# Kernel optimization log

Measured on AMD Instinct MI355X. Metric: run time of the kernel, lower is better.

The kernel has to match this reference:

```python
import jax, jax.numpy as jnp
import numpy as np

EMBED = 512
EXPAND = 1024


def setup_inputs() -> dict:
    key = jax.random.key(0)
    k1, k2, k3, k4, k5 = jax.random.split(key, 5)
    B, C, P, N = 4, EMBED, 16, 1024
    x = jax.random.normal(k1, (B, C, P, N), dtype=jnp.float32)
    # 1x1 conv weights == per-pixel linear maps over the channel dim
    Wqkv = jax.random.normal(k2, (1 + 2 * EXPAND, C), dtype=jnp.float32) * (1.0 / np.sqrt(C))
    bqkv = jax.random.normal(k3, (1 + 2 * EXPAND,), dtype=jnp.float32) * 0.01
    Wout = jax.random.normal(k4, (C, EXPAND), dtype=jnp.float32) * (1.0 / np.sqrt(EXPAND))
    bout = jax.random.normal(k5, (C,), dtype=jnp.float32) * 0.01
    return {"x": x, "Wqkv": Wqkv, "bqkv": bqkv, "Wout": Wout, "bout": bout}


def reference(x, Wqkv, bqkv, Wout, bout):
    # qkv 1x1 conv: (B,C,P,N) -> (B, 1+2E, P, N)
    qkv = jnp.einsum('oc,bcpn->bopn', Wqkv, x) + bqkv[None, :, None, None]
    E = EXPAND
    query = qkv[:, :1]            # (B,1,P,N)
    key_t = qkv[:, 1:1 + E]       # (B,E,P,N)
    value = qkv[:, 1 + E:]        # (B,E,P,N)
    # softmax over patches dim (last axis); attn_dropout p=0.0 -> identity
    context_scores = jax.nn.softmax(query, axis=-1)
    # weighted sum over N, keepdim -> (B,E,P,1)
    context_vector = jnp.sum(key_t * context_scores, axis=-1, keepdims=True)
    # broadcast gate
    out = jax.nn.relu(value) * context_vector  # (B,E,P,N)
    # out 1x1 conv back to embed channels
    out = jnp.einsum('oe,bepn->bopn', Wout, out) + bout[None, :, None, None]
    return out
```

## Files before the change

### kernel.cpp

```cpp
#include <hip/hip_runtime.h>

#define EMBED 512
#define EXPAND 1024
#define PNUM 16
#define NLEN 1024
#define CHW (PNUM * NLEN)
#define SLABS 64

typedef unsigned short u16;
typedef unsigned int u32;
typedef __bf16 bf16x8 __attribute__((ext_vector_type(8)));
typedef u16 u16x8 __attribute__((ext_vector_type(8)));
typedef float f32x4 __attribute__((ext_vector_type(4)));

__device__ __forceinline__ u16 f2bf(float f) {
  u32 u = __builtin_bit_cast(u32, f);
  return (u16)((u + 0x7FFFu + ((u >> 16) & 1u)) >> 16);
}
__device__ __forceinline__ float bf2f(u16 h) {
  return __builtin_bit_cast(float, (u32)h << 16);
}
__device__ __forceinline__ void gld16(const u16* g, u16* l) {
  __builtin_amdgcn_global_load_lds((__attribute__((address_space(1))) void*)g,
                                   (__attribute__((address_space(3))) void*)l,
                                   16, 0, 0);
}
__device__ __forceinline__ f32x4 MFMA(bf16x8 a, bf16x8 b, f32x4 c) {
  return __builtin_amdgcn_mfma_f32_16x16x32_bf16(a, b, c, 0, 0, 0);
}

__global__ __launch_bounds__(256) void k_convert_w(
    const float* __restrict__ Wqkv, const float* __restrict__ Wout,
    u16* __restrict__ WvB, u16* __restrict__ WoutB) {
  const int NV = EXPAND * EMBED;
  int idx = (blockIdx.x * 256 + threadIdx.x) * 4;
  if (idx < NV) {
    float4 v = *(const float4*)(Wqkv + (size_t)(1 + EXPAND) * EMBED + idx);
    uint2 u = make_uint2((u32)f2bf(v.x) | ((u32)f2bf(v.y) << 16),
                         (u32)f2bf(v.z) | ((u32)f2bf(v.w) << 16));
    *(uint2*)(WvB + idx) = u;
  } else {
    int j = idx - NV;
    float4 v = *(const float4*)(Wout + j);
    uint2 u = make_uint2((u32)f2bf(v.x) | ((u32)f2bf(v.y) << 16),
                         (u32)f2bf(v.z) | ((u32)f2bf(v.w) << 16));
    *(uint2*)(WoutB + j) = u;
  }
}

__global__ __launch_bounds__(256) void k_convert_x(
    const float* __restrict__ x, const float* __restrict__ Wqkv,
    float* __restrict__ q, u16* __restrict__ xbT) {
  __shared__ __align__(16) u16 tile[128 * 64];
  __shared__ float qp[256 * 4];
  const int slab = blockIdx.x >> 3, nw = blockIdx.x & 7;
  const int b = slab >> 4, p = slab & 15;
  const int t = threadIdx.x;
  const int c8 = t & 7;
  const int ng = t >> 3;
  const float* xs = x + (size_t)b * (EMBED * CHW) + (size_t)p * NLEN + nw * 128;
  u16* dst = xbT + (size_t)slab * (NLEN * EMBED) + (size_t)(nw * 128) * EMBED;
  float qa[4] = {0.f, 0.f, 0.f, 0.f};

  for (int cc = 0; cc < 8; ++cc) {
    const int cbase = cc * 64;
    float4 v[8];
#pragma unroll
    for (int k = 0; k < 8; ++k)
      v[k] = *(const float4*)(xs + (size_t)(cbase + c8 * 8 + k) * CHW + ng * 4);
    const float* w0 = Wqkv + cbase + c8 * 8;
#pragma unroll
    for (int k = 0; k < 8; ++k) {
      qa[0] += w0[k] * v[k].x;
      qa[1] += w0[k] * v[k].y;
      qa[2] += w0[k] * v[k].z;
      qa[3] += w0[k] * v[k].w;
    }
#pragma unroll
    for (int j = 0; j < 4; ++j) {
      const int nl = ng * 4 + j;
      float e[8];
#pragma unroll
      for (int k = 0; k < 8; ++k)
        e[k] = (j == 0) ? v[k].x : (j == 1) ? v[k].y : (j == 2) ? v[k].z : v[k].w;
      uint4 pk;
      pk.x = (u32)f2bf(e[0]) | ((u32)f2bf(e[1]) << 16);
      pk.y = (u32)f2bf(e[2]) | ((u32)f2bf(e[3]) << 16);
      pk.z = (u32)f2bf(e[4]) | ((u32)f2bf(e[5]) << 16);
      pk.w = (u32)f2bf(e[6]) | ((u32)f2bf(e[7]) << 16);
      *(uint4*)(tile + nl * 64 + ((c8 ^ (nl & 7)) << 3)) = pk;
    }
    __syncthreads();
#pragma unroll
    for (int m = 0; m < 4; ++m) {
      const int s = m * 256 + t;
      const int nl = s >> 3, ch = s & 7;
      uint4 vv = *(const uint4*)(tile + nl * 64 + ((ch ^ (nl & 7)) << 3));
      *(uint4*)(dst + (size_t)nl * EMBED + cbase + ch * 8) = vv;
    }
    __syncthreads();
  }
  qp[t * 4 + 0] = qa[0];
  qp[t * 4 + 1] = qa[1];
  qp[t * 4 + 2] = qa[2];
  qp[t * 4 + 3] = qa[3];
  __syncthreads();
  if (t < 128) {
    float a = 0.f;
#pragma unroll
    for (int o = 0; o < 8; ++o) a += qp[((((t >> 2) << 3) + o) << 2) + (t & 3)];
    q[(size_t)slab * NLEN + nw * 128 + t] = a;
  }
}

__global__ __launch_bounds__(256) void k_attn1(
    const float* __restrict__ q, const u16* __restrict__ xbT,
    float* __restrict__ ypart) {
  __shared__ float red[4];
  __shared__ float sm[256];
  __shared__ float yp[4][512];
  const int slab = blockIdx.x >> 2, qr = blockIdx.x & 3;
  const int t = threadIdx.x, w = t >> 6, l = t & 63;
  const float* qrow = q + (size_t)slab * NLEN;

  float4 q4 = ((const float4*)qrow)[t];
  float m = fmaxf(fmaxf(q4.x, q4.y), fmaxf(q4.z, q4.w));
#pragma unroll
  for (int sh = 32; sh; sh >>= 1) m = fmaxf(m, __shfl_xor(m, sh, 64));
  if (l == 0) red[w] = m;
  __syncthreads();
  float gm = fmaxf(fmaxf(red[0], red[1]), fmaxf(red[2], red[3]));
  float s = __expf(q4.x - gm) + __expf(q4.y - gm) + __expf(q4.z - gm) + __expf(q4.w - gm);
#pragma unroll
  for (int sh = 32; sh; sh >>= 1) s += __shfl_xor(s, sh, 64);
  __syncthreads();
  if (l == 0) red[w] = s;
  __syncthreads();
  float gs = red[0] + red[1] + red[2] + red[3];
  sm[t] = __expf(qrow[qr * 256 + t] - gm) / gs;
  __syncthreads();

  float ya[8] = {0.f, 0.f, 0.f, 0.f, 0.f, 0.f, 0.f, 0.f};
  const u16* xs = xbT + (size_t)slab * (NLEN * EMBED) + (size_t)qr * 256 * EMBED;
  for (int ni = 0; ni < 64; ++ni) {
    const int nloc = ni * 4 + w;
    const float sc = sm[nloc];
    u16x8 v = *(const u16x8*)(xs + (size_t)nloc * EMBED + l * 8);
#pragma unroll
    for (int j = 0; j < 8; ++j) ya[j] += sc * bf2f(v[j]);
  }
#pragma unroll
  for (int j = 0; j < 8; ++j) yp[w][l * 8 + j] = ya[j];
  __syncthreads();
  for (int c = t; c < 512; c += 256)
    ypart[((size_t)slab * 4 + qr) * 512 + c] = yp[0][c] + yp[1][c] + yp[2][c] + yp[3][c];
}

__global__ __launch_bounds__(256) void k_attn2(
    const float* __restrict__ ypart, const float* __restrict__ Wqkv,
    const float* __restrict__ bqkv, float* __restrict__ cv) {
  __shared__ float yl[512];
  const int slab = blockIdx.x >> 2, ec = blockIdx.x & 3;
  const int t = threadIdx.x;
  const int e = ec * 256 + t;
  const float* yb = ypart + (size_t)slab * 4 * 512;
  for (int c = t; c < 512; c += 256)
    yl[c] = yb[c] + yb[512 + c] + yb[1024 + c] + yb[1536 + c];
  __syncthreads();
  const float* wk = Wqkv + (size_t)(1 + e) * EMBED;
  float a = 0.f;
#pragma unroll 4
  for (int c0 = 0; c0 < EMBED; c0 += 4) {
    float4 wv = *(const float4*)(wk + c0);
    a += wv.x * yl[c0] + wv.y * yl[c0 + 1] + wv.z * yl[c0 + 2] + wv.w * yl[c0 + 3];
  }
  cv[(size_t)slab * EXPAND + e] = a + bqkv[1 + e];
}

template <int K, int NT>
__device__ __forceinline__ void gemm256(const u16* __restrict__ Abase,
                                        const u16* __restrict__ Bbase,
                                        u16* lds, f32x4 (&acc)[8][4]) {
  const int t = threadIdx.x;
  const int w = t >> 6, l = t & 63;
  const int wr = w >> 2, wc = w & 3;
  const int lr = l & 15, lj = l >> 4;
  const int rowA0 = wr * 128 + lr;
  const int rowB0 = wc * 64 + lr;

  auto stage = [&](u16* dstBase, const u16* gBase, int kt) {
#pragma unroll
    for (int i = 0; i < 4; ++i) {
      const int s = i * 512 + t;
      const int row = s >> 3;
      const int pch = s & 7;
      gld16(gBase + (size_t)row * K + kt + ((pch ^ (row & 7)) << 3),
            dstBase + s * 8);
    }
  };
  auto rdA = [&](const u16* bufA, int mi, int kc) -> bf16x8 {
    const int row = rowA0 + mi * 16;
    const int ch = kc * 4 + lj;
    return *(const bf16x8*)(bufA + row * 64 + ((ch ^ (row & 7)) << 3));
  };
  auto rdB = [&](const u16* bufB, int ni, int kc) -> bf16x8 {
    const int row = rowB0 + ni * 16;
    const int ch = kc * 4 + lj;
    return *(const bf16x8*)(bufB + row * 64 + ((ch ^ (row & 7)) << 3));
  };

  stage(lds, Abase, 0);
  stage(lds + 16384, Bbase, 0);
  stage(lds + 32768, Abase, 64);
  stage(lds + 49152, Bbase, 64);
  asm volatile("s_waitcnt vmcnt(8)" ::: "memory");
  __builtin_amdgcn_s_barrier();
  __builtin_amdgcn_sched_barrier(0);

#pragma unroll 1
  for (int kt = 0; kt < NT; ++kt) {
    u16* bufA = lds + (kt & 1) * 32768;
    u16* bufB = bufA + 16384;
    const bool st = (kt + 2) < NT;
    const int kt2 = (kt + 2) * 64;
    bf16x8 a0[4][2], a1[4][2], b0[2][2], b1[2][2];

#pragma unroll
    for (int mi = 0; mi < 4; ++mi)
#pragma unroll
      for (int kc = 0; kc < 2; ++kc) a0[mi][kc] = rdA(bufA, mi, kc);
#pragma unroll
    for (int ni = 0; ni < 2; ++ni)
#pragma unroll
      for (int kc = 0; kc < 2; ++kc) b0[ni][kc] = rdB(bufB, ni, kc);
    __builtin_amdgcn_s_barrier();
    __builtin_amdgcn_sched_barrier(0);
    __builtin_amdgcn_s_setprio(1);
#pragma unroll
    for (int mi = 0; mi < 4; ++mi)
#pragma unroll
      for (int ni = 0; ni < 2; ++ni)
#pragma unroll
        for (int kc = 0; kc < 2; ++kc)
          acc[mi][ni] = MFMA(a0[mi][kc], b0[ni][kc], acc[mi][ni]);
    __builtin_amdgcn_s_setprio(0);
    __builtin_amdgcn_sched_barrier(0);
    __builtin_amdgcn_s_barrier();
    __builtin_amdgcn_sched_barrier(0);

#pragma unroll
    for (int ni = 0; ni < 2; ++ni)
#pragma unroll
      for (int kc = 0; kc < 2; ++kc) b1[ni][kc] = rdB(bufB, ni + 2, kc);
    __builtin_amdgcn_s_barrier();
    __builtin_amdgcn_sched_barrier(0);
    __builtin_amdgcn_s_setprio(1);
#pragma unroll
    for (int mi = 0; mi < 4; ++mi)
#pragma unroll
      for (int ni = 0; ni < 2; ++ni)
#pragma unroll
        for (int kc = 0; kc < 2; ++kc)
          acc[mi][ni + 2] = MFMA(a0[mi][kc], b1[ni][kc], acc[mi][ni + 2]);
    __builtin_amdgcn_s_setprio(0);
    __builtin_amdgcn_sched_barrier(0);
    __builtin_amdgcn_s_barrier();
    __builtin_amdgcn_sched_barrier(0);

#pragma unroll
    for (int mi = 0; mi < 4; ++mi)
#pragma unroll
      for (int kc = 0; kc < 2; ++kc) a1[mi][kc] = rdA(bufA, mi + 4, kc);
    if (st) stage(bufB, Bbase, kt2);
    __builtin_amdgcn_s_barrier();
    __builtin_amdgcn_sched_barrier(0);
    __builtin_amdgcn_s_setprio(1);
#pragma unroll
    for (int mi = 0; mi < 4; ++mi)
#pragma unroll
      for (int ni = 0; ni < 2; ++ni)
#pragma unroll
        for (int kc = 0; kc < 2; ++kc)
          acc[mi + 4][ni + 2] = MFMA(a1[mi][kc], b1[ni][kc], acc[mi + 4][ni + 2]);
    __builtin_amdgcn_s_setprio(0);
    __builtin_amdgcn_sched_barrier(0);
    __builtin_amdgcn_s_barrier();
    __builtin_amdgcn_sched_barrier(0);

    if (st) stage(bufA, Abase, kt2);
    __builtin_amdgcn_s_barrier();
    __builtin_amdgcn_sched_barrier(0);
    __builtin_amdgcn_s_setprio(1);
#pragma unroll
    for (int mi = 0; mi < 4; ++mi)
#pragma unroll
      for (int ni = 0; ni < 2; ++ni)
#pragma unroll
        for (int kc = 0; kc < 2; ++kc)
          acc[mi + 4][ni] = MFMA(a1[mi][kc], b0[ni][kc], acc[mi + 4][ni]);
    __builtin_amdgcn_s_setprio(0);
    __builtin_amdgcn_sched_barrier(0);
    if (st)
      asm volatile("s_waitcnt vmcnt(8)" ::: "memory");
    else
      asm volatile("s_waitcnt vmcnt(0)" ::: "memory");
    __builtin_amdgcn_s_barrier();
    __builtin_amdgcn_sched_barrier(0);
  }
}

__global__ __launch_bounds__(512, 2) void k_gemm1(
    const u16* __restrict__ xbT, const u16* __restrict__ WvB,
    const float* __restrict__ bqkv, const float* __restrict__ cv,
    u16* __restrict__ midT) {
  __shared__ __align__(16) u16 lds[65536];
  const int bid = blockIdx.x;
  const int xc = bid & 7, k = bid >> 3;
  const int te = k & 3;
  const int gg = ((k >> 2) << 3) | xc;
  const int slab = gg >> 2, tn = gg & 3;
  const u16* A = xbT + (size_t)slab * (NLEN * EMBED) + (size_t)tn * 256 * EMBED;
  const u16* B = WvB + (size_t)te * 256 * EMBED;
  f32x4 acc[8][4];
  const f32x4 z = {0.f, 0.f, 0.f, 0.f};
#pragma unroll
  for (int i = 0; i < 8; ++i)
#pragma unroll
    for (int j = 0; j < 4; ++j) acc[i][j] = z;
  gemm256<EMBED, 8>(A, B, lds, acc);

  const int t = threadIdx.x, w = t >> 6, l = t & 63;
  const int wr = w >> 2, wc = w & 3;
  const int lr = l & 15, lq4 = (l >> 4) * 4;
#pragma unroll
  for (int ni = 0; ni < 4; ++ni) {
    const int col = wc * 64 + ni * 16 + lr;
    const int e = te * 256 + col;
    const float bv = bqkv[1 + EXPAND + e];
    const float cve = cv[(size_t)slab * EXPAND + e];
#pragma unroll
    for (int mi = 0; mi < 8; ++mi) {
      const int nr = wr * 128 + mi * 16 + lq4;
#pragma unroll
      for (int r = 0; r < 4; ++r) {
        float v = acc[mi][ni][r] + bv;
        v = v > 0.f ? v * cve : 0.f;
        const int row = nr + r;
        lds[row * 256 + ((((col >> 3) ^ (row & 7)) << 3) | (col & 7))] = f2bf(v);
      }
    }
  }
  __syncthreads();
  u16* mt = midT + (size_t)slab * (NLEN * EXPAND) + (size_t)te * 256;
#pragma unroll
  for (int it = 0; it < 16; ++it) {
    const int row = w * 32 + it * 2 + (l >> 5);
    const int ch = (l & 31) ^ (row & 7);
    uint4 v = *(const uint4*)(lds + row * 256 + ch * 8);
    *(uint4*)(mt + (size_t)(tn * 256 + row) * EXPAND + (l & 31) * 8) = v;
  }
}

__global__ __launch_bounds__(512, 2) void k_gemm2(
    const u16* __restrict__ midT, const u16* __restrict__ WoutB,
    const float* __restrict__ bout, float* __restrict__ out) {
  __shared__ __align__(16) u16 lds[65536];
  const int bid = blockIdx.x;
  const int xc = bid & 7, k = bid >> 3;
  const int to = k & 1;
  const int gg = ((k >> 1) << 3) | xc;
  const int slab = gg >> 2, tn = gg & 3;
  const int b = slab >> 4, p = slab & 15;
  const u16* A = midT + (size_t)slab * (NLEN * EXPAND) + (size_t)tn * 256 * EXPAND;
  const u16* B = WoutB + (size_t)to * 256 * EXPAND;
  f32x4 acc[8][4];
  const f32x4 z = {0.f, 0.f, 0.f, 0.f};
#pragma unroll
  for (int i = 0; i < 8; ++i)
#pragma unroll
    for (int j = 0; j < 4; ++j) acc[i][j] = z;
  gemm256<EXPAND, 16>(A, B, lds, acc);

  const int t = threadIdx.x, w = t >> 6, l = t & 63;
  const int wr = w >> 2, wc = w & 3;
  const int lr = l & 15, lq4 = (l >> 4) * 4;
  float* ob = out + (size_t)b * (EMBED * CHW) + (size_t)p * NLEN;
#pragma unroll
  for (int ni = 0; ni < 4; ++ni) {
    const int o = to * 256 + wc * 64 + ni * 16 + lr;
    const float bo = bout[o];
#pragma unroll
    for (int mi = 0; mi < 8; ++mi) {
      const int nr = tn * 256 + wr * 128 + mi * 16 + lq4;
      float4 v;
      v.x = acc[mi][ni][0] + bo;
      v.y = acc[mi][ni][1] + bo;
      v.z = acc[mi][ni][2] + bo;
      v.w = acc[mi][ni][3] + bo;
      *(float4*)(ob + (size_t)o * CHW + nr) = v;
    }
  }
}

extern "C" void kernel_launch(void* const* d_in, const int* in_sizes, int n_in,
                              void* d_out, int out_size, void* d_ws, size_t ws_size,
                              hipStream_t stream) {
  const float* x = (const float*)d_in[0];
  const float* Wqkv = (const float*)d_in[1];
  const float* bqkv = (const float*)d_in[2];
  const float* Wout = (const float*)d_in[3];
  const float* bout = (const float*)d_in[4];
  float* out = (float*)d_out;

  char* ws = (char*)d_ws;
  u16* xbT = (u16*)ws;
  u16* WvB = (u16*)(ws + 67108864);
  u16* WoutB = (u16*)(ws + 68157440);
  float* q = (float*)(ws + 69206016);
  float* cv = (float*)(ws + 69468160);
  u16* midT = (u16*)(ws + 69730304);
  float* ypart = (float*)(ws + 69730304);

  k_convert_w<<<1024, 256, 0, stream>>>(Wqkv, Wout, WvB, WoutB);
  k_convert_x<<<512, 256, 0, stream>>>(x, Wqkv, q, xbT);
  k_attn1<<<256, 256, 0, stream>>>(q, xbT, ypart);
  k_attn2<<<256, 256, 0, stream>>>(ypart, Wqkv, bqkv, cv);
  k_gemm1<<<1024, 512, 0, stream>>>(xbT, WvB, bqkv, cv, midT);
  k_gemm2<<<512, 512, 0, stream>>>(midT, WoutB, bout, out);
}
```

Before: 267.7 us.

## Switch GEMMs to 32x32x16 MFMA with swapped operands and direct epilogue stores

Both bf16 GEMMs move from the 16x16x32 to the 32x32x16 MFMA instruction, so each wave holds four 32x32 accumulator blocks instead of thirty-two 16x16 blocks. The weight matrix becomes operand A and the activations operand B, which removes the LDS transpose and the extra barrier in gemm1's epilogue. gemm1 now writes midT directly with small strided stores, and gemm2 writes the output row by row with coalesced scalar stores. Weight conversion is moved after attn1 so it can reuse the q buffer for a copy of the value bias, and several sched_barriers are dropped. The risk is less coalesced global writes in gemm1's epilogue and looser instruction scheduling.

```diff
diff --git a/kernel.cpp b/kernel.cpp
--- a/kernel.cpp
+++ b/kernel.cpp
@@ -12,6 +12,7 @@
 typedef __bf16 bf16x8 __attribute__((ext_vector_type(8)));
 typedef u16 u16x8 __attribute__((ext_vector_type(8)));
 typedef float f32x4 __attribute__((ext_vector_type(4)));
+typedef float f32x16 __attribute__((ext_vector_type(16)));
 
 __device__ __forceinline__ u16 f2bf(float f) {
   u32 u = __builtin_bit_cast(u32, f);
@@ -25,13 +26,14 @@
                                    (__attribute__((address_space(3))) void*)l,
                                    16, 0, 0);
 }
-__device__ __forceinline__ f32x4 MFMA(bf16x8 a, bf16x8 b, f32x4 c) {
-  return __builtin_amdgcn_mfma_f32_16x16x32_bf16(a, b, c, 0, 0, 0);
+__device__ __forceinline__ f32x16 MFMA32(bf16x8 a, bf16x8 b, f32x16 c) {
+  return __builtin_amdgcn_mfma_f32_32x32x16_bf16(a, b, c, 0, 0, 0);
 }
 
 __global__ __launch_bounds__(256) void k_convert_w(
     const float* __restrict__ Wqkv, const float* __restrict__ Wout,
-    u16* __restrict__ WvB, u16* __restrict__ WoutB) {
+    const float* __restrict__ bqkv, u16* __restrict__ WvB,
+    u16* __restrict__ WoutB, float* __restrict__ bvv) {
   const int NV = EXPAND * EMBED;
   int idx = (blockIdx.x * 256 + threadIdx.x) * 4;
   if (idx < NV) {
@@ -46,6 +48,10 @@
                          (u32)f2bf(v.z) | ((u32)f2bf(v.w) << 16));
     *(uint2*)(WoutB + j) = u;
   }
+  if (blockIdx.x == 0) {
+    for (int i = threadIdx.x; i < EXPAND; i += 256)
+      bvv[i] = bqkv[1 + EXPAND + i];
+  }
 }
 
 __global__ __launch_bounds__(256) void k_convert_x(
@@ -180,33 +186,29 @@
 template <int K, int NT>
 __device__ __forceinline__ void gemm256(const u16* __restrict__ Abase,
                                         const u16* __restrict__ Bbase,
-                                        u16* lds, f32x4 (&acc)[8][4]) {
+                                        u16* lds, f32x16 (&acc)[4][2]) {
   const int t = threadIdx.x;
   const int w = t >> 6, l = t & 63;
   const int wr = w >> 2, wc = w & 3;
-  const int lr = l & 15, lj = l >> 4;
-  const int rowA0 = wr * 128 + lr;
-  const int rowB0 = wc * 64 + lr;
-
-  auto stage = [&](u16* dstBase, const u16* gBase, int kt) {
+  const int l31 = l & 31, lh = l >> 5;
+
+  auto stage = [&](u16* dst, const u16* g, int kt) {
 #pragma unroll
     for (int i = 0; i < 4; ++i) {
       const int s = i * 512 + t;
-      const int row = s >> 3;
-      const int pch = s & 7;
-      gld16(gBase + (size_t)row * K + kt + ((pch ^ (row & 7)) << 3),
-            dstBase + s * 8);
+      const int row = s >> 3, pch = s & 7;
+      gld16(g + (size_t)row * K + kt + ((pch ^ (row & 7)) << 3), dst + s * 8);
     }
   };
-  auto rdA = [&](const u16* bufA, int mi, int kc) -> bf16x8 {
-    const int row = rowA0 + mi * 16;
-    const int ch = kc * 4 + lj;
-    return *(const bf16x8*)(bufA + row * 64 + ((ch ^ (row & 7)) << 3));
+  auto rdA = [&](const u16* buf, int mb, int ks) -> bf16x8 {
+    const int row = wr * 128 + mb * 32 + l31;
+    const int ch = ks * 2 + lh;
+    return *(const bf16x8*)(buf + row * 64 + ((ch ^ (row & 7)) << 3));
   };
-  auto rdB = [&](const u16* bufB, int ni, int kc) -> bf16x8 {
-    const int row = rowB0 + ni * 16;
-    const int ch = kc * 4 + lj;
-    return *(const bf16x8*)(bufB + row * 64 + ((ch ^ (row & 7)) << 3));
+  auto rdB = [&](const u16* buf, int nb, int ks) -> bf16x8 {
+    const int row = wc * 64 + nb * 32 + l31;
+    const int ch = ks * 2 + lh;
+    return *(const bf16x8*)(buf + row * 64 + ((ch ^ (row & 7)) << 3));
   };
 
   stage(lds, Abase, 0);
@@ -215,103 +217,78 @@
   stage(lds + 49152, Bbase, 64);
   asm volatile("s_waitcnt vmcnt(8)" ::: "memory");
   __builtin_amdgcn_s_barrier();
-  __builtin_amdgcn_sched_barrier(0);
 
 #pragma unroll 1
   for (int kt = 0; kt < NT; ++kt) {
     u16* bufA = lds + (kt & 1) * 32768;
     u16* bufB = bufA + 16384;
     const bool st = (kt + 2) < NT;
-    const int kt2 = (kt + 2) * 64;
-    bf16x8 a0[4][2], a1[4][2], b0[2][2], b1[2][2];
-
-#pragma unroll
-    for (int mi = 0; mi < 4; ++mi)
-#pragma unroll
-      for (int kc = 0; kc < 2; ++kc) a0[mi][kc] = rdA(bufA, mi, kc);
-#pragma unroll
-    for (int ni = 0; ni < 2; ++ni)
-#pragma unroll
-      for (int kc = 0; kc < 2; ++kc) b0[ni][kc] = rdB(bufB, ni, kc);
-    __builtin_amdgcn_s_barrier();
-    __builtin_amdgcn_sched_barrier(0);
+    const int k2 = (kt + 2) * 64;
+    bf16x8 a0[2][4], a1[2][4], b0[4], b1[4];
+
+#pragma unroll
+    for (int mb = 0; mb < 2; ++mb)
+#pragma unroll
+      for (int ks = 0; ks < 4; ++ks) a0[mb][ks] = rdA(bufA, mb, ks);
+#pragma unroll
+    for (int ks = 0; ks < 4; ++ks) b0[ks] = rdB(bufB, 0, ks);
+    __builtin_amdgcn_s_barrier();
     __builtin_amdgcn_s_setprio(1);
 #pragma unroll
-    for (int mi = 0; mi < 4; ++mi)
-#pragma unroll
-      for (int ni = 0; ni < 2; ++ni)
-#pragma unroll
-        for (int kc = 0; kc < 2; ++kc)
-          acc[mi][ni] = MFMA(a0[mi][kc], b0[ni][kc], acc[mi][ni]);
+    for (int mb = 0; mb < 2; ++mb)
+#pragma unroll
+      for (int ks = 0; ks < 4; ++ks)
+        acc[mb][0] = MFMA32(a0[mb][ks], b0[ks], acc[mb][0]);
     __builtin_amdgcn_s_setprio(0);
-    __builtin_amdgcn_sched_barrier(0);
-    __builtin_amdgcn_s_barrier();
-    __builtin_amdgcn_sched_barrier(0);
-
-#pragma unroll
-    for (int ni = 0; ni < 2; ++ni)
-#pragma unroll
-      for (int kc = 0; kc < 2; ++kc) b1[ni][kc] = rdB(bufB, ni + 2, kc);
-    __builtin_amdgcn_s_barrier();
-    __builtin_amdgcn_sched_barrier(0);
+    __builtin_amdgcn_s_barrier();
+
+#pragma unroll
+    for (int ks = 0; ks < 4; ++ks) b1[ks] = rdB(bufB, 1, ks);
+    __builtin_amdgcn_s_barrier();
     __builtin_amdgcn_s_setprio(1);
 #pragma unroll
-    for (int mi = 0; mi < 4; ++mi)
-#pragma unroll
-      for (int ni = 0; ni < 2; ++ni)
-#pragma unroll
-        for (int kc = 0; kc < 2; ++kc)
-          acc[mi][ni + 2] = MFMA(a0[mi][kc], b1[ni][kc], acc[mi][ni + 2]);
+    for (int mb = 0; mb < 2; ++mb)
+#pragma unroll
+      for (int ks = 0; ks < 4; ++ks)
+        acc[mb][1] = MFMA32(a0[mb][ks], b1[ks], acc[mb][1]);
     __builtin_amdgcn_s_setprio(0);
-    __builtin_amdgcn_sched_barrier(0);
-    __builtin_amdgcn_s_barrier();
-    __builtin_amdgcn_sched_barrier(0);
-
-#pragma unroll
-    for (int mi = 0; mi < 4; ++mi)
-#pragma unroll
-      for (int kc = 0; kc < 2; ++kc) a1[mi][kc] = rdA(bufA, mi + 4, kc);
-    if (st) stage(bufB, Bbase, kt2);
-    __builtin_amdgcn_s_barrier();
-    __builtin_amdgcn_sched_barrier(0);
+    __builtin_amdgcn_s_barrier();
+
+#pragma unroll
+    for (int mb = 0; mb < 2; ++mb)
+#pragma unroll
+      for (int ks = 0; ks < 4; ++ks) a1[mb][ks] = rdA(bufA, mb + 2, ks);
+    if (st) stage(bufB, Bbase, k2);
+    __builtin_amdgcn_s_barrier();
     __builtin_amdgcn_s_setprio(1);
 #pragma unroll
-    for (int mi = 0; mi < 4; ++mi)
-#pragma unroll
-      for (int ni = 0; ni < 2; ++ni)
-#pragma unroll
-        for (int kc = 0; kc < 2; ++kc)
-          acc[mi + 4][ni + 2] = MFMA(a1[mi][kc], b1[ni][kc], acc[mi + 4][ni + 2]);
+    for (int mb = 0; mb < 2; ++mb)
+#pragma unroll
+      for (int ks = 0; ks < 4; ++ks)
+        acc[mb + 2][1] = MFMA32(a1[mb][ks], b1[ks], acc[mb + 2][1]);
     __builtin_amdgcn_s_setprio(0);
-    __builtin_amdgcn_sched_barrier(0);
-    __builtin_amdgcn_s_barrier();
-    __builtin_amdgcn_sched_barrier(0);
-
-    if (st) stage(bufA, Abase, kt2);
-    __builtin_amdgcn_s_barrier();
-    __builtin_amdgcn_sched_barrier(0);
+    __builtin_amdgcn_s_barrier();
+
+    if (st) stage(bufA, Abase, k2);
+    __builtin_amdgcn_s_barrier();
     __builtin_amdgcn_s_setprio(1);
 #pragma unroll
-    for (int mi = 0; mi < 4; ++mi)
-#pragma unroll
-      for (int ni = 0; ni < 2; ++ni)
-#pragma unroll
-        for (int kc = 0; kc < 2; ++kc)
-          acc[mi + 4][ni] = MFMA(a1[mi][kc], b0[ni][kc], acc[mi + 4][ni]);
+    for (int mb = 0; mb < 2; ++mb)
+#pragma unroll
+      for (int ks = 0; ks < 4; ++ks)
+        acc[mb + 2][0] = MFMA32(a1[mb][ks], b0[ks], acc[mb + 2][0]);
     __builtin_amdgcn_s_setprio(0);
-    __builtin_amdgcn_sched_barrier(0);
     if (st)
       asm volatile("s_waitcnt vmcnt(8)" ::: "memory");
     else
       asm volatile("s_waitcnt vmcnt(0)" ::: "memory");
     __builtin_amdgcn_s_barrier();
-    __builtin_amdgcn_sched_barrier(0);
   }
 }
 
 __global__ __launch_bounds__(512, 2) void k_gemm1(
     const u16* __restrict__ xbT, const u16* __restrict__ WvB,
-    const float* __restrict__ bqkv, const float* __restrict__ cv,
+    const float* __restrict__ bvv, const float* __restrict__ cv,
     u16* __restrict__ midT) {
   __shared__ __align__(16) u16 lds[65536];
   const int bid = blockIdx.x;
@@ -319,45 +296,41 @@
   const int te = k & 3;
   const int gg = ((k >> 2) << 3) | xc;
   const int slab = gg >> 2, tn = gg & 3;
-  const u16* A = xbT + (size_t)slab * (NLEN * EMBED) + (size_t)tn * 256 * EMBED;
-  const u16* B = WvB + (size_t)te * 256 * EMBED;
-  f32x4 acc[8][4];
-  const f32x4 z = {0.f, 0.f, 0.f, 0.f};
-#pragma unroll
-  for (int i = 0; i < 8; ++i)
-#pragma unroll
-    for (int j = 0; j < 4; ++j) acc[i][j] = z;
+  const u16* A = WvB + (size_t)te * (256 * EMBED);
+  const u16* B = xbT + (size_t)slab * (NLEN * EMBED) + (size_t)tn * 256 * EMBED;
+  f32x16 acc[4][2];
+#pragma unroll
+  for (int i = 0; i < 4; ++i)
+#pragma unroll
+    for (int j = 0; j < 2; ++j)
+#pragma unroll
+      for (int r = 0; r < 16; ++r) acc[i][j][r] = 0.f;
   gemm256<EMBED, 8>(A, B, lds, acc);
 
   const int t = threadIdx.x, w = t >> 6, l = t & 63;
   const int wr = w >> 2, wc = w & 3;
-  const int lr = l & 15, lq4 = (l >> 4) * 4;
-#pragma unroll
-  for (int ni = 0; ni < 4; ++ni) {
-    const int col = wc * 64 + ni * 16 + lr;
-    const int e = te * 256 + col;
-    const float bv = bqkv[1 + EXPAND + e];
-    const float cve = cv[(size_t)slab * EXPAND + e];
-#pragma unroll
-    for (int mi = 0; mi < 8; ++mi) {
-      const int nr = wr * 128 + mi * 16 + lq4;
-#pragma unroll
-      for (int r = 0; r < 4; ++r) {
-        float v = acc[mi][ni][r] + bv;
-        v = v > 0.f ? v * cve : 0.f;
-        const int row = nr + r;
-        lds[row * 256 + ((((col >> 3) ^ (row & 7)) << 3) | (col & 7))] = f2bf(v);
+  const int l31 = l & 31, lh = l >> 5;
+  u16* mt = midT + (size_t)slab * (NLEN * EXPAND);
+#pragma unroll
+  for (int nb = 0; nb < 2; ++nb) {
+    const int n = tn * 256 + wc * 64 + nb * 32 + l31;
+#pragma unroll
+    for (int mb = 0; mb < 4; ++mb) {
+#pragma unroll
+      for (int rg = 0; rg < 4; ++rg) {
+        const int e0 = te * 256 + wr * 128 + mb * 32 + rg * 8 + lh * 4;
+        const float4 cv4 = *(const float4*)(cv + (size_t)slab * EXPAND + e0);
+        const float4 bv4 = *(const float4*)(bvv + e0);
+        float v0 = acc[mb][nb][rg * 4 + 0] + bv4.x; v0 = v0 > 0.f ? v0 * cv4.x : 0.f;
+        float v1 = acc[mb][nb][rg * 4 + 1] + bv4.y; v1 = v1 > 0.f ? v1 * cv4.y : 0.f;
+        float v2 = acc[mb][nb][rg * 4 + 2] + bv4.z; v2 = v2 > 0.f ? v2 * cv4.z : 0.f;
+        float v3 = acc[mb][nb][rg * 4 + 3] + bv4.w; v3 = v3 > 0.f ? v3 * cv4.w : 0.f;
+        uint2 pk;
+        pk.x = (u32)f2bf(v0) | ((u32)f2bf(v1) << 16);
+        pk.y = (u32)f2bf(v2) | ((u32)f2bf(v3) << 16);
+        *(uint2*)(mt + (size_t)n * EXPAND + e0) = pk;
       }
     }
-  }
-  __syncthreads();
-  u16* mt = midT + (size_t)slab * (NLEN * EXPAND) + (size_t)te * 256;
-#pragma unroll
-  for (int it = 0; it < 16; ++it) {
-    const int row = w * 32 + it * 2 + (l >> 5);
-    const int ch = (l & 31) ^ (row & 7);
-    uint4 v = *(const uint4*)(lds + row * 256 + ch * 8);
-    *(uint4*)(mt + (size_t)(tn * 256 + row) * EXPAND + (l & 31) * 8) = v;
   }
 }
 
@@ -371,33 +344,35 @@
   const int gg = ((k >> 1) << 3) | xc;
   const int slab = gg >> 2, tn = gg & 3;
   const int b = slab >> 4, p = slab & 15;
-  const u16* A = midT + (size_t)slab * (NLEN * EXPAND) + (size_t)tn * 256 * EXPAND;
-  const u16* B = WoutB + (size_t)to * 256 * EXPAND;
-  f32x4 acc[8][4];
-  const f32x4 z = {0.f, 0.f, 0.f, 0.f};
-#pragma unroll
-  for (int i = 0; i < 8; ++i)
-#pragma unroll
-    for (int j = 0; j < 4; ++j) acc[i][j] = z;
+  const u16* A = WoutB + (size_t)to * (256 * EXPAND);
+  const u16* B = midT + (size_t)slab * (NLEN * EXPAND) + (size_t)tn * 256 * EXPAND;
+  f32x16 acc[4][2];
+#pragma unroll
+  for (int i = 0; i < 4; ++i)
+#pragma unroll
+    for (int j = 0; j < 2; ++j)
+#pragma unroll
+      for (int r = 0; r < 16; ++r) acc[i][j][r] = 0.f;
   gemm256<EXPAND, 16>(A, B, lds, acc);
 
   const int t = threadIdx.x, w = t >> 6, l = t & 63;
   const int wr = w >> 2, wc = w & 3;
-  const int lr = l & 15, lq4 = (l >> 4) * 4;
+  const int l31 = l & 31, lh = l >> 5;
   float* ob = out + (size_t)b * (EMBED * CHW) + (size_t)p * NLEN;
 #pragma unroll
-  for (int ni = 0; ni < 4; ++ni) {
-    const int o = to * 256 + wc * 64 + ni * 16 + lr;
-    const float bo = bout[o];
-#pragma unroll
-    for (int mi = 0; mi < 8; ++mi) {
-      const int nr = tn * 256 + wr * 128 + mi * 16 + lq4;
-      float4 v;
-      v.x = acc[mi][ni][0] + bo;
-      v.y = acc[mi][ni][1] + bo;
-      v.z = acc[mi][ni][2] + bo;
-      v.w = acc[mi][ni][3] + bo;
-      *(float4*)(ob + (size_t)o * CHW + nr) = v;
+  for (int nb = 0; nb < 2; ++nb) {
+    const int n = tn * 256 + wc * 64 + nb * 32 + l31;
+#pragma unroll
+    for (int mb = 0; mb < 4; ++mb) {
+#pragma unroll
+      for (int rg = 0; rg < 4; ++rg) {
+        const int o0 = to * 256 + wr * 128 + mb * 32 + rg * 8 + lh * 4;
+        const float4 bo4 = *(const float4*)(bout + o0);
+        ob[(size_t)(o0 + 0) * CHW + n] = acc[mb][nb][rg * 4 + 0] + bo4.x;
+        ob[(size_t)(o0 + 1) * CHW + n] = acc[mb][nb][rg * 4 + 1] + bo4.y;
+        ob[(size_t)(o0 + 2) * CHW + n] = acc[mb][nb][rg * 4 + 2] + bo4.z;
+        ob[(size_t)(o0 + 3) * CHW + n] = acc[mb][nb][rg * 4 + 3] + bo4.w;
+      }
     }
   }
 }
@@ -420,11 +395,12 @@
   float* cv = (float*)(ws + 69468160);
   u16* midT = (u16*)(ws + 69730304);
   float* ypart = (float*)(ws + 69730304);
-
-  k_convert_w<<<1024, 256, 0, stream>>>(Wqkv, Wout, WvB, WoutB);
+  float* bvv = (float*)(ws + 69206016);
+
   k_convert_x<<<512, 256, 0, stream>>>(x, Wqkv, q, xbT);
   k_attn1<<<256, 256, 0, stream>>>(q, xbT, ypart);
+  k_convert_w<<<1024, 256, 0, stream>>>(Wqkv, Wout, bqkv, WvB, WoutB, bvv);
   k_attn2<<<256, 256, 0, stream>>>(ypart, Wqkv, bqkv, cv);
-  k_gemm1<<<1024, 512, 0, stream>>>(xbT, WvB, bqkv, cv, midT);
+  k_gemm1<<<1024, 512, 0, stream>>>(xbT, WvB, bvv, cv, midT);
   k_gemm2<<<512, 512, 0, stream>>>(midT, WoutB, bout, out);
 }
```

New measurement: 312.3 us. 1.17x slower.
